# Kernel tuning notes

Measured on AMD Instinct MI355X. Metric: run time of the kernel, lower is better.

The kernel has to match this reference:

```python
import jax, jax.numpy as jnp
import numpy as np
import math

B, S, E, H, DK, DV = 2, 2048, 1024, 16, 64, 64
EPS = 1e-06


def setup_inputs() -> dict:
    key = jax.random.key(0)
    ks = jax.random.split(key, 11)
    s_in = 1.0 / math.sqrt(E)
    return {
        "query": jax.random.normal(ks[0], (B, S, E), jnp.float32),
        "key_in": jax.random.normal(ks[1], (B, S, E), jnp.float32),
        "value_in": jax.random.normal(ks[2], (B, S, E), jnp.float32),
        "residual_x": jax.random.normal(ks[3], (B, S, E), jnp.float32),
        # stacked per-head Linear params (torch Linear: y = x @ W.T + b); here W stored as [H, E, d]
        "Wq": jax.random.uniform(ks[4], (H, E, DK), jnp.float32, -s_in, s_in),
        "bq": jax.random.uniform(ks[5], (H, DK), jnp.float32, -s_in, s_in),
        "Wk": jax.random.uniform(ks[6], (H, E, DK), jnp.float32, -s_in, s_in),
        "bk": jax.random.uniform(ks[7], (H, DK), jnp.float32, -s_in, s_in),
        "Wv": jax.random.uniform(ks[8], (H, E, DV), jnp.float32, -s_in, s_in),
        "bv": jax.random.uniform(ks[9], (H, DV), jnp.float32, -s_in, s_in),
        "ln_scale": jnp.ones((E,), jnp.float32),
        "ln_shift": jnp.zeros((E,), jnp.float32),
    }


def reference(query, key_in, value_in, residual_x, Wq, bq, Wk, bk, Wv, bv, ln_scale, ln_shift):
    # batched per-head projections (replaces python loop over heads)
    q = jnp.einsum("bse,hed->bhsd", query, Wq) + bq[None, :, None, :]
    k = jnp.einsum("bse,hed->bhsd", key_in, Wk) + bk[None, :, None, :]
    v = jnp.einsum("bse,hed->bhsd", value_in, Wv) + bv[None, :, None, :]
    scores = jnp.einsum("bhsd,bhtd->bhst", q, k) / math.sqrt(DK)  # [B,H,S,S]
    causal = jnp.tril(jnp.ones((S, S), bool))  # mask strictly-upper triangle to -inf
    scores = jnp.where(causal[None, None], scores, -jnp.inf)
    attn = jax.nn.softmax(scores, axis=-1)
    out = jnp.einsum("bhst,bhtd->bhsd", attn, v)
    # concat heads along feature dim (head order = cat order)
    out = out.transpose(0, 2, 1, 3).reshape(B, S, H * DV)
    x = out + residual_x
    # custom LayerNorm: unbiased std, shift added into denominator
    mean = x.mean(-1, keepdims=True)
    std = jnp.sqrt(jnp.sum((x - mean) ** 2, axis=-1, keepdims=True) / (E - 1))
    div = std + EPS + ln_shift  # broadcasts [B,S,1]+[E] -> [B,S,E]
    return ln_scale * (x - mean) / div
```

## Files before the change

### kernel.cpp

```cpp
#include <hip/hip_runtime.h>
#include <hip/hip_bf16.h>

#define NB 2
#define NS 2048
#define NE 1024
#define NH 16
#define ND 64
#define MTOT (NB * NS)

#define QSCALE 0.18033688011112042f

typedef __attribute__((ext_vector_type(8))) short bf8_t;
typedef __attribute__((ext_vector_type(4))) short bf4_t;
typedef __attribute__((ext_vector_type(4))) float f32x4;
typedef __attribute__((ext_vector_type(16))) float f32x16;

__device__ __forceinline__ short f2bf(float f) {
    union { float f; unsigned u; } v; v.f = f;
    return (short)((v.u + 0x7FFFu + ((v.u >> 16) & 1u)) >> 16);
}

__device__ __forceinline__ unsigned cvtpk(float lo, float hi) {
    unsigned r;
    asm("v_cvt_pk_bf16_f32 %0, %1, %2" : "=v"(r) : "v"(lo), "v"(hi));
    return r;
}

__device__ __forceinline__ bf8_t mk4(unsigned a, unsigned b, unsigned c, unsigned d) {
    union { unsigned u[4]; bf8_t v; } t;
    t.u[0] = a; t.u[1] = b; t.u[2] = c; t.u[3] = d;
    return t.v;
}

#define GLOAD16(g, l) __builtin_amdgcn_global_load_lds( \
    (const __attribute__((address_space(1))) void*)(g), \
    (__attribute__((address_space(3))) void*)(l), 16, 0, 0)

__global__ __launch_bounds__(256) void conv_kernel(
    const float* __restrict__ src, short* __restrict__ out)
{
    const size_t nchunk = (size_t)MTOT * NE / 8;
    const size_t stride = (size_t)gridDim.x * 256;
    for (size_t i = (size_t)blockIdx.x * 256 + threadIdx.x; i < nchunk; i += stride) {
        size_t e = i * 8;
        float4 x0 = *(const float4*)(src + e);
        float4 x1 = *(const float4*)(src + e + 4);
        bf8_t o;
        o[0] = f2bf(x0.x); o[1] = f2bf(x0.y); o[2] = f2bf(x0.z); o[3] = f2bf(x0.w);
        o[4] = f2bf(x1.x); o[5] = f2bf(x1.y); o[6] = f2bf(x1.z); o[7] = f2bf(x1.w);
        *(bf8_t*)(out + e) = o;
    }
}

__global__ __launch_bounds__(256) void wt_kernel(
    const float* __restrict__ Wq, const float* __restrict__ Wk, const float* __restrict__ Wv,
    short* __restrict__ wt)
{
    const int p = blockIdx.x / NH, h = blockIdx.x % NH;
    const int e0 = blockIdx.y * 64;
    const float* W = (p == 0) ? Wq : (p == 1) ? Wk : Wv;
    const int t = threadIdx.x;
    const int er = t >> 2, dc = (t & 3) * 16;
    const float* src = W + ((size_t)h * NE + e0 + er) * ND + dc;
    short* dst = wt + (size_t)(p * NH + h) * ND * NE;
#pragma unroll
    for (int j = 0; j < 16; j += 4) {
        float4 x = *(const float4*)(src + j);
        dst[(size_t)(dc + j + 0) * NE + e0 + er] = f2bf(x.x);
        dst[(size_t)(dc + j + 1) * NE + e0 + er] = f2bf(x.y);
        dst[(size_t)(dc + j + 2) * NE + e0 + er] = f2bf(x.z);
        dst[(size_t)(dc + j + 3) * NE + e0 + er] = f2bf(x.w);
    }
}

__global__ __launch_bounds__(256) void proj_kernel(
    const short* __restrict__ in_bf, const short* __restrict__ wt,
    const float* __restrict__ bq, const float* __restrict__ bk, const float* __restrict__ bv,
    short* __restrict__ q_ws, short* __restrict__ k_ws, short* __restrict__ vT_ws,
    int pbase)
{
    __shared__ __attribute__((aligned(16))) short As[128 * 32];
    __shared__ __attribute__((aligned(16))) short Bs[128 * 32];

    const int z = blockIdx.z, p = pbase + z;
    const short* A = in_bf + (size_t)z * MTOT * NE;
    const short* Bm = wt + (size_t)p * NE * NE;
    const float* bias_all = (p == 0) ? bq : (p == 1) ? bk : bv;
    const float oscale = (p == 0) ? QSCALE : 1.0f;

    const int m0 = blockIdx.x * 128, n0 = blockIdx.y * 128;
    const int t = threadIdx.x, lane = t & 63, w = t >> 6;
    const int l15 = lane & 15, g = lane >> 4;
    const int wr = w >> 1, wc = w & 1;

    const int srow = t >> 2, scol = (t & 3) * 8;
    const short* ag = A + (size_t)(m0 + srow) * NE + scol;
    const short* bg = Bm + (size_t)(n0 + srow) * NE + scol;
    short* asl = As + t * 8;
    short* bsl = Bs + t * 8;

    f32x4 acc[4][4];
#pragma unroll
    for (int i = 0; i < 4; ++i)
#pragma unroll
        for (int j = 0; j < 4; ++j) acc[i][j] = (f32x4){0.f, 0.f, 0.f, 0.f};

    for (int k0 = 0; k0 < NE; k0 += 32) {
        __syncthreads();
        GLOAD16(ag + k0, asl);
        GLOAD16(ag + k0 + (size_t)64 * NE, asl + 2048);
        GLOAD16(bg + k0, bsl);
        GLOAD16(bg + k0 + (size_t)64 * NE, bsl + 2048);
        __syncthreads();
        bf8_t af[4], bfr[4];
#pragma unroll
        for (int mf = 0; mf < 4; ++mf)
            af[mf] = *(const bf8_t*)&As[(wr * 64 + mf * 16 + l15) * 32 + g * 8];
#pragma unroll
        for (int nf = 0; nf < 4; ++nf)
            bfr[nf] = *(const bf8_t*)&Bs[(wc * 64 + nf * 16 + l15) * 32 + g * 8];
#pragma unroll
        for (int mf = 0; mf < 4; ++mf)
#pragma unroll
            for (int nf = 0; nf < 4; ++nf)
                acc[mf][nf] = __builtin_amdgcn_mfma_f32_16x16x32_bf16(af[mf], bfr[nf], acc[mf][nf], 0, 0, 0);
    }

    const int h = (n0 + wc * 64) >> 6;
    const float* bias = bias_all + h * ND;

    if (p < 2) {
        short* outp = (p == 0) ? q_ws : k_ws;
#pragma unroll
        for (int mf = 0; mf < 4; ++mf) {
            const int m = m0 + wr * 64 + mf * 16 + g * 4;
            const int bb = m >> 11, s = m & (NS - 1);
#pragma unroll
            for (int nf = 0; nf < 4; ++nf) {
                const int d = nf * 16 + l15;
                const float bi = bias[d];
                short* op = outp + (((size_t)bb * NH + h) * NS + s) * ND + d;
#pragma unroll
                for (int r = 0; r < 4; ++r)
                    op[(size_t)r * ND] = f2bf((acc[mf][nf][r] + bi) * oscale);
            }
        }
    } else {
#pragma unroll
        for (int mf = 0; mf < 4; ++mf) {
            const int m = m0 + wr * 64 + mf * 16 + g * 4;
            const int bb = m >> 11, s = m & (NS - 1);
#pragma unroll
            for (int nf = 0; nf < 4; ++nf) {
                const int d = nf * 16 + l15;
                const float bi = bias[d];
                bf4_t pk;
#pragma unroll
                for (int r = 0; r < 4; ++r) pk[r] = f2bf(acc[mf][nf][r] + bi);
                *(bf4_t*)&vT_ws[(((size_t)bb * NH + h) * ND + d) * NS + s] = pk;
            }
        }
    }
}

__global__ __launch_bounds__(256, 2) void attn_kernel(
    const short* __restrict__ q_ws, const short* __restrict__ k_ws,
    const short* __restrict__ vT_ws, float* __restrict__ O)
{
    __shared__ float oT[4][32][65];
    const int t = threadIdx.x, lane = t & 63, w = t >> 6;
    const int g = (int)blockIdx.x * 4 + w;
    const int jq = 63 - (g >> 5);
    const int bh = g & 31;
    const int b = bh >> 4, h = bh & 15;
    const int q0w = jq * 32;
    const int nt = (jq >> 1) + 1;
    const int l31 = lane & 31, hi = lane >> 5;
    const size_t base = (size_t)bh * NS * ND;

    bf8_t Qf[4];
    {
        const short* qsrc = q_ws + base + (size_t)(q0w + l31) * ND + hi * 8;
#pragma unroll
        for (int s = 0; s < 4; ++s) Qf[s] = *(const bf8_t*)(qsrc + s * 16);
    }

    f32x16 Oa[2];
#pragma unroll
    for (int rb = 0; rb < 2; ++rb)
#pragma unroll
        for (int r = 0; r < 16; ++r) Oa[rb][r] = 0.f;
    float m_i = -1e30f, l_i = 0.f;
    const int qg = q0w + l31;

    for (int tt = 0; tt < nt; ++tt) {
        const int t0 = tt * 64;

        bf8_t Kf[2][4];
#pragma unroll
        for (int c = 0; c < 2; ++c) {
            const short* kp = k_ws + base + (size_t)(t0 + c * 32 + l31) * ND + hi * 8;
#pragma unroll
            for (int s = 0; s < 4; ++s) Kf[c][s] = *(const bf8_t*)(kp + s * 16);
        }
        bf8_t Vf[4][2];
#pragma unroll
        for (int rb = 0; rb < 2; ++rb) {
            const short* vp = vT_ws + base + (size_t)(rb * 32 + l31) * NS + t0 + hi * 8;
#pragma unroll
            for (int cs = 0; cs < 4; ++cs) Vf[cs][rb] = *(const bf8_t*)(vp + cs * 16);
        }

        f32x16 Sv[2];
#pragma unroll
        for (int c = 0; c < 2; ++c) {
#pragma unroll
            for (int r = 0; r < 16; ++r) Sv[c][r] = 0.f;
#pragma unroll
            for (int s = 0; s < 4; ++s)
                Sv[c] = __builtin_amdgcn_mfma_f32_32x32x16_bf16(Kf[c][s], Qf[s], Sv[c], 0, 0, 0);
        }

        if (tt == nt - 1) {
#pragma unroll
            for (int c = 0; c < 2; ++c)
#pragma unroll
                for (int r = 0; r < 16; ++r) {
                    const int kvg = t0 + c * 32 + (r & 3) + 8 * (r >> 2) + 4 * hi;
                    if (kvg > qg) Sv[c][r] = -1e30f;
                }
        }

        float mloc = Sv[0][0];
#pragma unroll
        for (int r = 1; r < 16; ++r) mloc = fmaxf(mloc, Sv[0][r]);
#pragma unroll
        for (int r = 0; r < 16; ++r) mloc = fmaxf(mloc, Sv[1][r]);
        mloc = fmaxf(mloc, __shfl_xor(mloc, 32));

        if (__any(mloc > m_i + 11.0f)) {
            const float mn = fmaxf(m_i, mloc);
            const float al = exp2f(m_i - mn);
            m_i = mn;
            l_i *= al;
#pragma unroll
            for (int rb = 0; rb < 2; ++rb)
#pragma unroll
                for (int r = 0; r < 16; ++r) Oa[rb][r] *= al;
        }

        float rs = 0.f;
        bf8_t Pf[2][2];
#pragma unroll
        for (int c = 0; c < 2; ++c) {
#pragma unroll
            for (int r = 0; r < 16; ++r) {
                const float pv = exp2f(Sv[c][r] - m_i);
                Sv[c][r] = pv;
                rs += pv;
            }
            unsigned wv[8], xv[8];
#pragma unroll
            for (int i = 0; i < 8; ++i) wv[i] = cvtpk(Sv[c][2 * i], Sv[c][2 * i + 1]);
#pragma unroll
            for (int i = 0; i < 8; ++i) xv[i] = __shfl_xor(wv[i], 32);
            Pf[c][0] = hi ? mk4(xv[2], xv[3], wv[2], wv[3]) : mk4(wv[0], wv[1], xv[0], xv[1]);
            Pf[c][1] = hi ? mk4(xv[6], xv[7], wv[6], wv[7]) : mk4(wv[4], wv[5], xv[4], xv[5]);
        }
        rs += __shfl_xor(rs, 32);
        l_i += rs;

#pragma unroll
        for (int cs = 0; cs < 4; ++cs)
#pragma unroll
            for (int rb = 0; rb < 2; ++rb)
                Oa[rb] = __builtin_amdgcn_mfma_f32_32x32x16_bf16(Vf[cs][rb], Pf[cs >> 1][cs & 1], Oa[rb], 0, 0, 0);
    }

    const float inv = 1.0f / l_i;
#pragma unroll
    for (int rb = 0; rb < 2; ++rb)
#pragma unroll
        for (int r = 0; r < 16; ++r)
            oT[w][l31][rb * 32 + (r & 3) + 8 * (r >> 2) + 4 * hi] = Oa[rb][r] * inv;

    asm volatile("s_waitcnt lgkmcnt(0)" ::: "memory");

#pragma unroll
    for (int p4 = 0; p4 < 4; ++p4) {
        const int qr = p4 * 8 + (lane >> 3), d8 = (lane & 7) * 8;
        const float4 a0 = *(const float4*)&oT[w][qr][d8];
        const float4 a1 = *(const float4*)&oT[w][qr][d8 + 4];
        float* op = O + ((size_t)b * NS + q0w + qr) * NE + h * 64 + d8;
        *(float4*)op = a0;
        *(float4*)(op + 4) = a1;
    }
}

__global__ __launch_bounds__(256) void ln_kernel(
    const float* __restrict__ Oin, const float* __restrict__ resid,
    const float* __restrict__ ln_scale, const float* __restrict__ ln_shift,
    float* __restrict__ out)
{
    __shared__ float red[8];
    const int row = blockIdx.x, t = threadIdx.x;
    const size_t basei = (size_t)row * NE + t * 4;
    float4 x = *(const float4*)(Oin + basei);
    float4 rr = *(const float4*)(resid + basei);
    x.x += rr.x; x.y += rr.y; x.z += rr.z; x.w += rr.w;
    float ps = x.x + x.y + x.z + x.w;
#pragma unroll
    for (int off = 32; off; off >>= 1) ps += __shfl_xor(ps, off);
    if ((t & 63) == 0) red[t >> 6] = ps;
    __syncthreads();
    const float mean = (red[0] + red[1] + red[2] + red[3]) * (1.0f / NE);
    const float dx0 = x.x - mean, dx1 = x.y - mean, dx2 = x.z - mean, dx3 = x.w - mean;
    float ss = dx0 * dx0 + dx1 * dx1 + dx2 * dx2 + dx3 * dx3;
#pragma unroll
    for (int off = 32; off; off >>= 1) ss += __shfl_xor(ss, off);
    if ((t & 63) == 0) red[4 + (t >> 6)] = ss;
    __syncthreads();
    const float stdv = sqrtf((red[4] + red[5] + red[6] + red[7]) * (1.0f / (NE - 1)));
    float4 sc = *(const float4*)(ln_scale + t * 4);
    float4 sh = *(const float4*)(ln_shift + t * 4);
    float4 o;
    o.x = sc.x * dx0 / (stdv + 1e-6f + sh.x);
    o.y = sc.y * dx1 / (stdv + 1e-6f + sh.y);
    o.z = sc.z * dx2 / (stdv + 1e-6f + sh.z);
    o.w = sc.w * dx3 / (stdv + 1e-6f + sh.w);
    *(float4*)(out + basei) = o;
}

extern "C" void kernel_launch(void* const* d_in, const int* in_sizes, int n_in,
                              void* d_out, int out_size, void* d_ws, size_t ws_size,
                              hipStream_t stream) {
    (void)in_sizes; (void)n_in; (void)out_size; (void)ws_size;
    const float* query    = (const float*)d_in[0];
    const float* key_in   = (const float*)d_in[1];
    const float* value_in = (const float*)d_in[2];
    const float* resid    = (const float*)d_in[3];
    const float* Wq = (const float*)d_in[4];
    const float* bq = (const float*)d_in[5];
    const float* Wk = (const float*)d_in[6];
    const float* bk = (const float*)d_in[7];
    const float* Wv = (const float*)d_in[8];
    const float* bv = (const float*)d_in[9];
    const float* ln_scale = (const float*)d_in[10];
    const float* ln_shift = (const float*)d_in[11];
    float* out = (float*)d_out;

    char* ws = (char*)d_ws;
    short* wt_ws = (short*)ws;
    short* in_bf = (short*)(ws + (6u << 20));
    short* q_ws  = (short*)(ws + (22u << 20));
    short* k_ws  = (short*)(ws + (30u << 20));
    short* vT_ws = (short*)(ws + (38u << 20));
    float* O_ws  = (float*)ws;

    short* slot0 = in_bf;
    short* slot1 = in_bf + (size_t)MTOT * NE;

    wt_kernel<<<dim3(3 * NH, NE / 64), 256, 0, stream>>>(Wq, Wk, Wv, wt_ws);

    conv_kernel<<<1024, 256, 0, stream>>>(query, slot0);
    conv_kernel<<<1024, 256, 0, stream>>>(key_in, slot1);
    proj_kernel<<<dim3(MTOT / 128, NE / 128, 2), 256, 0, stream>>>(
        in_bf, wt_ws, bq, bk, bv, q_ws, k_ws, vT_ws, 0);

    conv_kernel<<<1024, 256, 0, stream>>>(value_in, slot0);
    proj_kernel<<<dim3(MTOT / 128, NE / 128, 1), 256, 0, stream>>>(
        in_bf, wt_ws, bq, bk, bv, q_ws, k_ws, vT_ws, 2);

    attn_kernel<<<512, 256, 0, stream>>>(q_ws, k_ws, vT_ws, O_ws);
    ln_kernel<<<dim3(NB * NS), 256, 0, stream>>>(O_ws, resid, ln_scale, ln_shift, out);
}
```

Measured before the change: 285.0 us.

## Fuse input conversion into projection and split attention KV range across two waves

Removes the separate fp32-to-bf16 conversion kernels. The projection GEMM now loads fp32 activations straight into XOR-swizzled LDS and converts them while building fragments, and all three projections run in one launch. Attention splits each query tile's causal KV range into two halves, each in its own wave, to improve parallelism and load balance. Each half writes an unnormalized bf16 partial output plus its running max and sum, and the LayerNorm kernel merges the two halves before normalizing. This trades extra partial-output traffic, bf16 rounding of intermediates, and doubled fp32 LDS staging in the GEMM for fewer launches and better occupancy.

```diff
diff --git a/kernel.cpp b/kernel.cpp
--- a/kernel.cpp
+++ b/kernel.cpp
@@ -19,13 +19,15 @@
     union { float f; unsigned u; } v; v.f = f;
     return (short)((v.u + 0x7FFFu + ((v.u >> 16) & 1u)) >> 16);
 }
-
+__device__ __forceinline__ float b2f(short s) {
+    union { unsigned u; float f; } v; v.u = ((unsigned)(unsigned short)s) << 16;
+    return v.f;
+}
 __device__ __forceinline__ unsigned cvtpk(float lo, float hi) {
     unsigned r;
     asm("v_cvt_pk_bf16_f32 %0, %1, %2" : "=v"(r) : "v"(lo), "v"(hi));
     return r;
 }
-
 __device__ __forceinline__ bf8_t mk4(unsigned a, unsigned b, unsigned c, unsigned d) {
     union { unsigned u[4]; bf8_t v; } t;
     t.u[0] = a; t.u[1] = b; t.u[2] = c; t.u[3] = d;
@@ -35,22 +37,6 @@
 #define GLOAD16(g, l) __builtin_amdgcn_global_load_lds( \
     (const __attribute__((address_space(1))) void*)(g), \
     (__attribute__((address_space(3))) void*)(l), 16, 0, 0)
-
-__global__ __launch_bounds__(256) void conv_kernel(
-    const float* __restrict__ src, short* __restrict__ out)
-{
-    const size_t nchunk = (size_t)MTOT * NE / 8;
-    const size_t stride = (size_t)gridDim.x * 256;
-    for (size_t i = (size_t)blockIdx.x * 256 + threadIdx.x; i < nchunk; i += stride) {
-        size_t e = i * 8;
-        float4 x0 = *(const float4*)(src + e);
-        float4 x1 = *(const float4*)(src + e + 4);
-        bf8_t o;
-        o[0] = f2bf(x0.x); o[1] = f2bf(x0.y); o[2] = f2bf(x0.z); o[3] = f2bf(x0.w);
-        o[4] = f2bf(x1.x); o[5] = f2bf(x1.y); o[6] = f2bf(x1.z); o[7] = f2bf(x1.w);
-        *(bf8_t*)(out + e) = o;
-    }
-}
 
 __global__ __launch_bounds__(256) void wt_kernel(
     const float* __restrict__ Wq, const float* __restrict__ Wk, const float* __restrict__ Wv,
@@ -74,29 +60,32 @@
 }
 
 __global__ __launch_bounds__(256) void proj_kernel(
-    const short* __restrict__ in_bf, const short* __restrict__ wt,
+    const float* __restrict__ query, const float* __restrict__ key_in, const float* __restrict__ value_in,
+    const short* __restrict__ wt,
     const float* __restrict__ bq, const float* __restrict__ bk, const float* __restrict__ bv,
-    short* __restrict__ q_ws, short* __restrict__ k_ws, short* __restrict__ vT_ws,
-    int pbase)
+    short* __restrict__ q_ws, short* __restrict__ k_ws, short* __restrict__ vT_ws)
 {
-    __shared__ __attribute__((aligned(16))) short As[128 * 32];
+    __shared__ __attribute__((aligned(16))) float Asf[128 * 32];
     __shared__ __attribute__((aligned(16))) short Bs[128 * 32];
 
-    const int z = blockIdx.z, p = pbase + z;
-    const short* A = in_bf + (size_t)z * MTOT * NE;
+    const int p = blockIdx.z;
+    const float* A = (p == 0) ? query : (p == 1) ? key_in : value_in;
     const short* Bm = wt + (size_t)p * NE * NE;
     const float* bias_all = (p == 0) ? bq : (p == 1) ? bk : bv;
     const float oscale = (p == 0) ? QSCALE : 1.0f;
 
     const int m0 = blockIdx.x * 128, n0 = blockIdx.y * 128;
     const int t = threadIdx.x, lane = t & 63, w = t >> 6;
-    const int l15 = lane & 15, g = lane >> 4;
+    const int l15 = lane & 15, g = lane >> 4, g8 = g * 8;
     const int wr = w >> 1, wc = w & 1;
 
-    const int srow = t >> 2, scol = (t & 3) * 8;
-    const short* ag = A + (size_t)(m0 + srow) * NE + scol;
-    const short* bg = Bm + (size_t)(n0 + srow) * NE + scol;
-    short* asl = As + t * 8;
+    const int arow = t >> 3;
+    const int acol = ((t & 7) * 4) ^ ((arow & 3) << 3);
+    const float* ag = A + (size_t)(m0 + arow) * NE + acol;
+    float* asl = Asf + t * 4;
+    const int brow = t >> 2;
+    const int bcol = ((t & 3) * 8) ^ ((brow & 3) << 3);
+    const short* bg = Bm + (size_t)(n0 + brow) * NE + bcol;
     short* bsl = Bs + t * 8;
 
     f32x4 acc[4][4];
@@ -104,21 +93,34 @@
     for (int i = 0; i < 4; ++i)
 #pragma unroll
         for (int j = 0; j < 4; ++j) acc[i][j] = (f32x4){0.f, 0.f, 0.f, 0.f};
+
+    const int aswz = (l15 & 3) << 3;
 
     for (int k0 = 0; k0 < NE; k0 += 32) {
         __syncthreads();
         GLOAD16(ag + k0, asl);
+        GLOAD16(ag + k0 + (size_t)32 * NE, asl + 1024);
         GLOAD16(ag + k0 + (size_t)64 * NE, asl + 2048);
+        GLOAD16(ag + k0 + (size_t)96 * NE, asl + 3072);
         GLOAD16(bg + k0, bsl);
         GLOAD16(bg + k0 + (size_t)64 * NE, bsl + 2048);
         __syncthreads();
+
         bf8_t af[4], bfr[4];
 #pragma unroll
-        for (int mf = 0; mf < 4; ++mf)
-            af[mf] = *(const bf8_t*)&As[(wr * 64 + mf * 16 + l15) * 32 + g * 8];
-#pragma unroll
-        for (int nf = 0; nf < 4; ++nf)
-            bfr[nf] = *(const bf8_t*)&Bs[(wc * 64 + nf * 16 + l15) * 32 + g * 8];
+        for (int mf = 0; mf < 4; ++mf) {
+            const int ar = wr * 64 + mf * 16 + l15;
+            const float* ap = &Asf[ar * 32 + (g8 ^ aswz)];
+            f32x4 v0 = *(const f32x4*)ap;
+            f32x4 v1 = *(const f32x4*)(ap + 4);
+            af[mf] = mk4(cvtpk(v0[0], v0[1]), cvtpk(v0[2], v0[3]),
+                         cvtpk(v1[0], v1[1]), cvtpk(v1[2], v1[3]));
+        }
+#pragma unroll
+        for (int nf = 0; nf < 4; ++nf) {
+            const int br = wc * 64 + nf * 16 + l15;
+            bfr[nf] = *(const bf8_t*)&Bs[br * 32 + (g8 ^ aswz)];
+        }
 #pragma unroll
         for (int mf = 0; mf < 4; ++mf)
 #pragma unroll
@@ -163,18 +165,23 @@
     }
 }
 
-__global__ __launch_bounds__(256, 2) void attn_kernel(
+__global__ __launch_bounds__(256) void attn_kernel(
     const short* __restrict__ q_ws, const short* __restrict__ k_ws,
-    const short* __restrict__ vT_ws, float* __restrict__ O)
+    const short* __restrict__ vT_ws, short* __restrict__ oPart, float2* __restrict__ ml)
 {
-    __shared__ float oT[4][32][65];
+    __shared__ float oT[4][32][33];
     const int t = threadIdx.x, lane = t & 63, w = t >> 6;
-    const int g = (int)blockIdx.x * 4 + w;
-    const int jq = 63 - (g >> 5);
-    const int bh = g & 31;
+    const int jj = (int)blockIdx.x * 4 + w;
+    const int j2 = jj >> 5;
+    const int jq = 63 - (j2 >> 1);
+    const int half = j2 & 1;
+    const int bh = jj & 31;
     const int b = bh >> 4, h = bh & 15;
     const int q0w = jq * 32;
-    const int nt = (jq >> 1) + 1;
+    const int ntot = (jq >> 1) + 1;
+    const int mid = ntot >> 1;
+    const int ts = half ? mid : 0;
+    const int te = half ? ntot : mid;
     const int l31 = lane & 31, hi = lane >> 5;
     const size_t base = (size_t)bh * NS * ND;
 
@@ -193,7 +200,7 @@
     float m_i = -1e30f, l_i = 0.f;
     const int qg = q0w + l31;
 
-    for (int tt = 0; tt < nt; ++tt) {
+    for (int tt = ts; tt < te; ++tt) {
         const int t0 = tt * 64;
 
         bf8_t Kf[2][4];
@@ -221,7 +228,7 @@
                 Sv[c] = __builtin_amdgcn_mfma_f32_32x32x16_bf16(Kf[c][s], Qf[s], Sv[c], 0, 0, 0);
         }
 
-        if (tt == nt - 1) {
+        if (tt == ntot - 1) {
 #pragma unroll
             for (int c = 0; c < 2; ++c)
 #pragma unroll
@@ -277,37 +284,62 @@
                 Oa[rb] = __builtin_amdgcn_mfma_f32_32x32x16_bf16(Vf[cs][rb], Pf[cs >> 1][cs & 1], Oa[rb], 0, 0, 0);
     }
 
-    const float inv = 1.0f / l_i;
-#pragma unroll
-    for (int rb = 0; rb < 2; ++rb)
+    if (hi == 0) ml[((size_t)half * 32 + bh) * NS + qg] = (float2){m_i, l_i};
+
+    short* obase = oPart + (size_t)half * MTOT * NE;
+#pragma unroll
+    for (int rb = 0; rb < 2; ++rb) {
 #pragma unroll
         for (int r = 0; r < 16; ++r)
-            oT[w][l31][rb * 32 + (r & 3) + 8 * (r >> 2) + 4 * hi] = Oa[rb][r] * inv;
-
-    asm volatile("s_waitcnt lgkmcnt(0)" ::: "memory");
-
-#pragma unroll
-    for (int p4 = 0; p4 < 4; ++p4) {
-        const int qr = p4 * 8 + (lane >> 3), d8 = (lane & 7) * 8;
-        const float4 a0 = *(const float4*)&oT[w][qr][d8];
-        const float4 a1 = *(const float4*)&oT[w][qr][d8 + 4];
-        float* op = O + ((size_t)b * NS + q0w + qr) * NE + h * 64 + d8;
-        *(float4*)op = a0;
-        *(float4*)(op + 4) = a1;
+            oT[w][l31][(r & 3) + 8 * (r >> 2) + 4 * hi] = Oa[rb][r];
+        asm volatile("s_waitcnt lgkmcnt(0)" ::: "memory");
+        const int q = lane >> 1, dhalf = (lane & 1) * 16;
+        const float* src = &oT[w][q][dhalf];
+        float4 a0 = *(const float4*)(src);
+        float4 a1 = *(const float4*)(src + 4);
+        float4 a2 = *(const float4*)(src + 8);
+        float4 a3 = *(const float4*)(src + 12);
+        short* dst = obase + ((size_t)b * NS + q0w + q) * NE + h * 64 + rb * 32 + dhalf;
+        *(bf8_t*)dst = mk4(cvtpk(a0.x, a0.y), cvtpk(a0.z, a0.w), cvtpk(a1.x, a1.y), cvtpk(a1.z, a1.w));
+        *(bf8_t*)(dst + 8) = mk4(cvtpk(a2.x, a2.y), cvtpk(a2.z, a2.w), cvtpk(a3.x, a3.y), cvtpk(a3.z, a3.w));
+        asm volatile("s_waitcnt lgkmcnt(0)" ::: "memory");
     }
 }
 
 __global__ __launch_bounds__(256) void ln_kernel(
-    const float* __restrict__ Oin, const float* __restrict__ resid,
+    const short* __restrict__ oPart, const float2* __restrict__ ml,
+    const float* __restrict__ resid,
     const float* __restrict__ ln_scale, const float* __restrict__ ln_shift,
     float* __restrict__ out)
 {
     __shared__ float red[8];
+    __shared__ float wtab[16][2];
     const int row = blockIdx.x, t = threadIdx.x;
+    const int b = row >> 11, s = row & (NS - 1);
+
+    if (t < 16) {
+        const float2 a = ml[((size_t)b * 16 + t) * NS + s];
+        const float2 c = ml[((size_t)(32 + b * 16 + t)) * NS + s];
+        const float m = fmaxf(a.x, c.x);
+        const float w0 = exp2f(a.x - m), w1 = exp2f(c.x - m);
+        const float inv = 1.0f / (w0 * a.y + w1 * c.y);
+        wtab[t][0] = w0 * inv;
+        wtab[t][1] = w1 * inv;
+    }
+    __syncthreads();
+
+    const int h = t >> 4;
+    const float w0 = wtab[h][0], w1 = wtab[h][1];
     const size_t basei = (size_t)row * NE + t * 4;
-    float4 x = *(const float4*)(Oin + basei);
+    const bf4_t o0 = *(const bf4_t*)&oPart[basei];
+    const bf4_t o1 = *(const bf4_t*)&oPart[(size_t)MTOT * NE + basei];
     float4 rr = *(const float4*)(resid + basei);
-    x.x += rr.x; x.y += rr.y; x.z += rr.z; x.w += rr.w;
+    float4 x;
+    x.x = w0 * b2f(o0[0]) + w1 * b2f(o1[0]) + rr.x;
+    x.y = w0 * b2f(o0[1]) + w1 * b2f(o1[1]) + rr.y;
+    x.z = w0 * b2f(o0[2]) + w1 * b2f(o1[2]) + rr.z;
+    x.w = w0 * b2f(o0[3]) + w1 * b2f(o1[3]) + rr.w;
+
     float ps = x.x + x.y + x.z + x.w;
 #pragma unroll
     for (int off = 32; off; off >>= 1) ps += __shfl_xor(ps, off);
@@ -350,27 +382,16 @@
     float* out = (float*)d_out;
 
     char* ws = (char*)d_ws;
-    short* wt_ws = (short*)ws;
-    short* in_bf = (short*)(ws + (6u << 20));
-    short* q_ws  = (short*)(ws + (22u << 20));
-    short* k_ws  = (short*)(ws + (30u << 20));
-    short* vT_ws = (short*)(ws + (38u << 20));
-    float* O_ws  = (float*)ws;
-
-    short* slot0 = in_bf;
-    short* slot1 = in_bf + (size_t)MTOT * NE;
+    short* wt_ws  = (short*)ws;
+    float2* ml_ws = (float2*)ws;
+    short* q_ws   = (short*)(ws + (6u << 20));
+    short* k_ws   = (short*)(ws + (14u << 20));
+    short* vT_ws  = (short*)(ws + (22u << 20));
+    short* oPart  = (short*)(ws + (30u << 20));
 
     wt_kernel<<<dim3(3 * NH, NE / 64), 256, 0, stream>>>(Wq, Wk, Wv, wt_ws);
-
-    conv_kernel<<<1024, 256, 0, stream>>>(query, slot0);
-    conv_kernel<<<1024, 256, 0, stream>>>(key_in, slot1);
-    proj_kernel<<<dim3(MTOT / 128, NE / 128, 2), 256, 0, stream>>>(
-        in_bf, wt_ws, bq, bk, bv, q_ws, k_ws, vT_ws, 0);
-
-    conv_kernel<<<1024, 256, 0, stream>>>(value_in, slot0);
-    proj_kernel<<<dim3(MTOT / 128, NE / 128, 1), 256, 0, stream>>>(
-        in_bf, wt_ws, bq, bk, bv, q_ws, k_ws, vT_ws, 2);
-
-    attn_kernel<<<512, 256, 0, stream>>>(q_ws, k_ws, vT_ws, O_ws);
-    ln_kernel<<<dim3(NB * NS), 256, 0, stream>>>(O_ws, resid, ln_scale, ln_shift, out);
-}
+    proj_kernel<<<dim3(MTOT / 128, NE / 128, 3), 256, 0, stream>>>(
+        query, key_in, value_in, wt_ws, bq, bk, bv, q_ws, k_ws, vT_ws);
+    attn_kernel<<<1024, 256, 0, stream>>>(q_ws, k_ws, vT_ws, oPart, ml_ws);
+    ln_kernel<<<dim3(NB * NS), 256, 0, stream>>>(oPart, ml_ws, resid, ln_scale, ln_shift, out);
+}
```

Measured after the change: 279.2 us. 2.0% less time.

## Fuse fp32-to-bf16 input conversion into projection GEMM and split attention KV across waves

Applied to the files above, without the earlier changes.

The separate conv_kernel passes are removed: the projection GEMM now reads fp32 activations directly, converts them to bf16 in registers and stores them to LDS, and all three projections run in one launch. The attention kernel changes from one query tile per wave to one query tile per block, with the four waves splitting the KV tiles and then merging partial softmax states through LDS (split-K flash attention). This removes the extra round trip of bf16 inputs through memory, cuts kernel launches, and gives the attention grid four times as many blocks for better load balance. The cost is non-async A loads in the GEMM loop, an extra bf16 rounding of the partial outputs before the merge, and a block-wide sync in attention.

```diff
diff --git a/kernel.cpp b/kernel.cpp
--- a/kernel.cpp
+++ b/kernel.cpp
@@ -19,13 +19,19 @@
     union { float f; unsigned u; } v; v.f = f;
     return (short)((v.u + 0x7FFFu + ((v.u >> 16) & 1u)) >> 16);
 }
-
+__device__ __forceinline__ float bflo(unsigned u) {
+    union { unsigned u; float f; } v; v.u = u << 16;
+    return v.f;
+}
+__device__ __forceinline__ float bfhi(unsigned u) {
+    union { unsigned u; float f; } v; v.u = u & 0xFFFF0000u;
+    return v.f;
+}
 __device__ __forceinline__ unsigned cvtpk(float lo, float hi) {
     unsigned r;
     asm("v_cvt_pk_bf16_f32 %0, %1, %2" : "=v"(r) : "v"(lo), "v"(hi));
     return r;
 }
-
 __device__ __forceinline__ bf8_t mk4(unsigned a, unsigned b, unsigned c, unsigned d) {
     union { unsigned u[4]; bf8_t v; } t;
     t.u[0] = a; t.u[1] = b; t.u[2] = c; t.u[3] = d;
@@ -35,22 +41,6 @@
 #define GLOAD16(g, l) __builtin_amdgcn_global_load_lds( \
     (const __attribute__((address_space(1))) void*)(g), \
     (__attribute__((address_space(3))) void*)(l), 16, 0, 0)
-
-__global__ __launch_bounds__(256) void conv_kernel(
-    const float* __restrict__ src, short* __restrict__ out)
-{
-    const size_t nchunk = (size_t)MTOT * NE / 8;
-    const size_t stride = (size_t)gridDim.x * 256;
-    for (size_t i = (size_t)blockIdx.x * 256 + threadIdx.x; i < nchunk; i += stride) {
-        size_t e = i * 8;
-        float4 x0 = *(const float4*)(src + e);
-        float4 x1 = *(const float4*)(src + e + 4);
-        bf8_t o;
-        o[0] = f2bf(x0.x); o[1] = f2bf(x0.y); o[2] = f2bf(x0.z); o[3] = f2bf(x0.w);
-        o[4] = f2bf(x1.x); o[5] = f2bf(x1.y); o[6] = f2bf(x1.z); o[7] = f2bf(x1.w);
-        *(bf8_t*)(out + e) = o;
-    }
-}
 
 __global__ __launch_bounds__(256) void wt_kernel(
     const float* __restrict__ Wq, const float* __restrict__ Wk, const float* __restrict__ Wv,
@@ -74,29 +64,29 @@
 }
 
 __global__ __launch_bounds__(256) void proj_kernel(
-    const short* __restrict__ in_bf, const short* __restrict__ wt,
+    const float* __restrict__ query, const float* __restrict__ key_in, const float* __restrict__ value_in,
+    const short* __restrict__ wt,
     const float* __restrict__ bq, const float* __restrict__ bk, const float* __restrict__ bv,
-    short* __restrict__ q_ws, short* __restrict__ k_ws, short* __restrict__ vT_ws,
-    int pbase)
+    short* __restrict__ q_ws, short* __restrict__ k_ws, short* __restrict__ vT_ws)
 {
     __shared__ __attribute__((aligned(16))) short As[128 * 32];
     __shared__ __attribute__((aligned(16))) short Bs[128 * 32];
 
-    const int z = blockIdx.z, p = pbase + z;
-    const short* A = in_bf + (size_t)z * MTOT * NE;
+    const int p = blockIdx.z;
+    const float* A = (p == 0) ? query : (p == 1) ? key_in : value_in;
     const short* Bm = wt + (size_t)p * NE * NE;
     const float* bias_all = (p == 0) ? bq : (p == 1) ? bk : bv;
     const float oscale = (p == 0) ? QSCALE : 1.0f;
 
     const int m0 = blockIdx.x * 128, n0 = blockIdx.y * 128;
     const int t = threadIdx.x, lane = t & 63, w = t >> 6;
-    const int l15 = lane & 15, g = lane >> 4;
+    const int l15 = lane & 15, g = lane >> 4, g8 = g * 8;
     const int wr = w >> 1, wc = w & 1;
 
-    const int srow = t >> 2, scol = (t & 3) * 8;
-    const short* ag = A + (size_t)(m0 + srow) * NE + scol;
-    const short* bg = Bm + (size_t)(n0 + srow) * NE + scol;
-    short* asl = As + t * 8;
+    const int arow = t >> 1, ac = (t & 1) * 16;
+    const float* ag = A + (size_t)(m0 + arow) * NE + ac;
+    short* awr = &As[arow * 32 + ac];
+    const short* bg = Bm + (size_t)(n0 + (t >> 2)) * NE + (t & 3) * 8;
     short* bsl = Bs + t * 8;
 
     f32x4 acc[4][4];
@@ -106,19 +96,26 @@
         for (int j = 0; j < 4; ++j) acc[i][j] = (f32x4){0.f, 0.f, 0.f, 0.f};
 
     for (int k0 = 0; k0 < NE; k0 += 32) {
+        const float4 x0 = *(const float4*)(ag + k0);
+        const float4 x1 = *(const float4*)(ag + k0 + 4);
+        const float4 x2 = *(const float4*)(ag + k0 + 8);
+        const float4 x3 = *(const float4*)(ag + k0 + 12);
         __syncthreads();
-        GLOAD16(ag + k0, asl);
-        GLOAD16(ag + k0 + (size_t)64 * NE, asl + 2048);
         GLOAD16(bg + k0, bsl);
         GLOAD16(bg + k0 + (size_t)64 * NE, bsl + 2048);
+        *(bf8_t*)awr = mk4(cvtpk(x0.x, x0.y), cvtpk(x0.z, x0.w),
+                           cvtpk(x1.x, x1.y), cvtpk(x1.z, x1.w));
+        *(bf8_t*)(awr + 8) = mk4(cvtpk(x2.x, x2.y), cvtpk(x2.z, x2.w),
+                                 cvtpk(x3.x, x3.y), cvtpk(x3.z, x3.w));
         __syncthreads();
+
         bf8_t af[4], bfr[4];
 #pragma unroll
         for (int mf = 0; mf < 4; ++mf)
-            af[mf] = *(const bf8_t*)&As[(wr * 64 + mf * 16 + l15) * 32 + g * 8];
+            af[mf] = *(const bf8_t*)&As[(wr * 64 + mf * 16 + l15) * 32 + g8];
 #pragma unroll
         for (int nf = 0; nf < 4; ++nf)
-            bfr[nf] = *(const bf8_t*)&Bs[(wc * 64 + nf * 16 + l15) * 32 + g * 8];
+            bfr[nf] = *(const bf8_t*)&Bs[(wc * 64 + nf * 16 + l15) * 32 + g8];
 #pragma unroll
         for (int mf = 0; mf < 4; ++mf)
 #pragma unroll
@@ -163,18 +160,20 @@
     }
 }
 
-__global__ __launch_bounds__(256, 2) void attn_kernel(
+__global__ __launch_bounds__(256) void attn_kernel(
     const short* __restrict__ q_ws, const short* __restrict__ k_ws,
     const short* __restrict__ vT_ws, float* __restrict__ O)
 {
-    __shared__ float oT[4][32][65];
+    __shared__ float cm[4][32], cl[4][32];
+    __shared__ __attribute__((aligned(16))) unsigned oP[4][32][36];
+
     const int t = threadIdx.x, lane = t & 63, w = t >> 6;
-    const int g = (int)blockIdx.x * 4 + w;
-    const int jq = 63 - (g >> 5);
-    const int bh = g & 31;
+    const int jj = (int)blockIdx.x;
+    const int jq = 63 - (jj >> 5);
+    const int bh = jj & 31;
     const int b = bh >> 4, h = bh & 15;
     const int q0w = jq * 32;
-    const int nt = (jq >> 1) + 1;
+    const int ntot = (jq >> 1) + 1;
     const int l31 = lane & 31, hi = lane >> 5;
     const size_t base = (size_t)bh * NS * ND;
 
@@ -193,7 +192,7 @@
     float m_i = -1e30f, l_i = 0.f;
     const int qg = q0w + l31;
 
-    for (int tt = 0; tt < nt; ++tt) {
+    for (int tt = w; tt < ntot; tt += 4) {
         const int t0 = tt * 64;
 
         bf8_t Kf[2][4];
@@ -221,7 +220,7 @@
                 Sv[c] = __builtin_amdgcn_mfma_f32_32x32x16_bf16(Kf[c][s], Qf[s], Sv[c], 0, 0, 0);
         }
 
-        if (tt == nt - 1) {
+        if (tt == ntot - 1) {
 #pragma unroll
             for (int c = 0; c < 2; ++c)
 #pragma unroll
@@ -277,23 +276,46 @@
                 Oa[rb] = __builtin_amdgcn_mfma_f32_32x32x16_bf16(Vf[cs][rb], Pf[cs >> 1][cs & 1], Oa[rb], 0, 0, 0);
     }
 
-    const float inv = 1.0f / l_i;
+    if (hi == 0) { cm[w][l31] = m_i; cl[w][l31] = l_i; }
 #pragma unroll
     for (int rb = 0; rb < 2; ++rb)
 #pragma unroll
-        for (int r = 0; r < 16; ++r)
-            oT[w][l31][rb * 32 + (r & 3) + 8 * (r >> 2) + 4 * hi] = Oa[rb][r] * inv;
-
-    asm volatile("s_waitcnt lgkmcnt(0)" ::: "memory");
-
-#pragma unroll
-    for (int p4 = 0; p4 < 4; ++p4) {
-        const int qr = p4 * 8 + (lane >> 3), d8 = (lane & 7) * 8;
-        const float4 a0 = *(const float4*)&oT[w][qr][d8];
-        const float4 a1 = *(const float4*)&oT[w][qr][d8 + 4];
-        float* op = O + ((size_t)b * NS + q0w + qr) * NE + h * 64 + d8;
-        *(float4*)op = a0;
-        *(float4*)(op + 4) = a1;
+        for (int q4 = 0; q4 < 4; ++q4) {
+            const int dp = rb * 16 + 4 * q4 + 2 * hi;
+            oP[w][l31][dp]     = cvtpk(Oa[rb][q4 * 4 + 0], Oa[rb][q4 * 4 + 1]);
+            oP[w][l31][dp + 1] = cvtpk(Oa[rb][q4 * 4 + 2], Oa[rb][q4 * 4 + 3]);
+        }
+    __syncthreads();
+
+    {
+        const int q = t >> 3, dp0 = (t & 7) * 4;
+        float wgt[4];
+        float mfin = fmaxf(fmaxf(cm[0][q], cm[1][q]), fmaxf(cm[2][q], cm[3][q]));
+        float lfin = 0.f;
+#pragma unroll
+        for (int ww = 0; ww < 4; ++ww) {
+            const float e = exp2f(cm[ww][q] - mfin);
+            lfin += e * cl[ww][q];
+            wgt[ww] = e;
+        }
+        const float inv = 1.0f / lfin;
+#pragma unroll
+        for (int ww = 0; ww < 4; ++ww) wgt[ww] *= inv;
+
+        float o[8];
+#pragma unroll
+        for (int j = 0; j < 8; ++j) o[j] = 0.f;
+#pragma unroll
+        for (int ww = 0; ww < 4; ++ww) {
+            const uint4 u = *(const uint4*)&oP[ww][q][dp0];
+            o[0] += wgt[ww] * bflo(u.x); o[1] += wgt[ww] * bfhi(u.x);
+            o[2] += wgt[ww] * bflo(u.y); o[3] += wgt[ww] * bfhi(u.y);
+            o[4] += wgt[ww] * bflo(u.z); o[5] += wgt[ww] * bfhi(u.z);
+            o[6] += wgt[ww] * bflo(u.w); o[7] += wgt[ww] * bfhi(u.w);
+        }
+        float* op = O + ((size_t)b * NS + q0w + q) * NE + h * 64 + dp0 * 2;
+        *(float4*)op = (float4){o[0], o[1], o[2], o[3]};
+        *(float4*)(op + 4) = (float4){o[4], o[5], o[6], o[7]};
     }
 }
 
@@ -351,26 +373,14 @@
 
     char* ws = (char*)d_ws;
     short* wt_ws = (short*)ws;
-    short* in_bf = (short*)(ws + (6u << 20));
-    short* q_ws  = (short*)(ws + (22u << 20));
-    short* k_ws  = (short*)(ws + (30u << 20));
-    short* vT_ws = (short*)(ws + (38u << 20));
-    float* O_ws  = (float*)ws;
-
-    short* slot0 = in_bf;
-    short* slot1 = in_bf + (size_t)MTOT * NE;
+    short* q_ws  = (short*)(ws + (6u << 20));
+    short* k_ws  = (short*)(ws + (14u << 20));
+    short* vT_ws = (short*)(ws + (22u << 20));
+    float* O_ws  = (float*)(ws + (30u << 20));
 
     wt_kernel<<<dim3(3 * NH, NE / 64), 256, 0, stream>>>(Wq, Wk, Wv, wt_ws);
-
-    conv_kernel<<<1024, 256, 0, stream>>>(query, slot0);
-    conv_kernel<<<1024, 256, 0, stream>>>(key_in, slot1);
-    proj_kernel<<<dim3(MTOT / 128, NE / 128, 2), 256, 0, stream>>>(
-        in_bf, wt_ws, bq, bk, bv, q_ws, k_ws, vT_ws, 0);
-
-    conv_kernel<<<1024, 256, 0, stream>>>(value_in, slot0);
-    proj_kernel<<<dim3(MTOT / 128, NE / 128, 1), 256, 0, stream>>>(
-        in_bf, wt_ws, bq, bk, bv, q_ws, k_ws, vT_ws, 2);
-
-    attn_kernel<<<512, 256, 0, stream>>>(q_ws, k_ws, vT_ws, O_ws);
+    proj_kernel<<<dim3(MTOT / 128, NE / 128, 3), 256, 0, stream>>>(
+        query, key_in, value_in, wt_ws, bq, bk, bv, q_ws, k_ws, vT_ws);
+    attn_kernel<<<2048, 256, 0, stream>>>(q_ws, k_ws, vT_ws, O_ws);
     ln_kernel<<<dim3(NB * NS), 256, 0, stream>>>(O_ws, resid, ln_scale, ln_shift, out);
 }
```

After: 286.4 us. Within noise of the previous version (+0.5%).
